# Kernel optimization log

Hardware: AMD Instinct MI355X
Metric: run time of the kernel (lower is better)

## Reference

```python
import jax, jax.numpy as jnp
import numpy as np

HIDDEN = 4096
N_HEADS = 32
N_KV_HEADS = 8
HEAD_DIM = 128
ROPE_BASE = 10000.0


def setup_inputs() -> dict:
    key = jax.random.key(0)
    k1, k2, k3, k4, k5 = jax.random.split(key, 5)
    s = 0.02  # init scale for weights
    return {
        "hidden_states": jax.random.normal(k1, (1, 2048, HIDDEN), dtype=jnp.float32),
        "Wq": jax.random.normal(k2, (N_HEADS * HEAD_DIM, HIDDEN), dtype=jnp.float32) * s,
        "Wk": jax.random.normal(k3, (N_KV_HEADS * HEAD_DIM, HIDDEN), dtype=jnp.float32) * s,
        "Wv": jax.random.normal(k4, (N_KV_HEADS * HEAD_DIM, HIDDEN), dtype=jnp.float32) * s,
        "Wo": jax.random.normal(k5, (HIDDEN, HIDDEN), dtype=jnp.float32) * s,
    }


def _rope(x, cos, sin):
    # x: [B, H, T, D]; cos/sin: [T, D/2] -> rotate split halves (Llama style)
    d2 = x.shape[-1] // 2
    x1, x2 = x[..., :d2], x[..., d2:]
    return jnp.concatenate([x1 * cos - x2 * sin, x1 * sin + x2 * cos], axis=-1)


def reference(hidden_states, Wq, Wk, Wv, Wo):
    B, T, _ = hidden_states.shape
    H, Hkv, D = N_HEADS, N_KV_HEADS, HEAD_DIM
    G = H // Hkv  # kv groups

    q = jnp.einsum("bth,qh->btq", hidden_states, Wq).reshape(B, T, H, D).transpose(0, 2, 1, 3)
    k = jnp.einsum("bth,kh->btk", hidden_states, Wk).reshape(B, T, Hkv, D).transpose(0, 2, 1, 3)
    v = jnp.einsum("bth,vh->btv", hidden_states, Wv).reshape(B, T, Hkv, D).transpose(0, 2, 1, 3)

    # RoPE (position_offset = 0)
    positions = jnp.arange(T, dtype=jnp.float32)
    inv_freq = ROPE_BASE ** (-jnp.arange(0, D, 2, dtype=jnp.float32) / D)  # [D/2]
    angles = positions[:, None] * inv_freq[None, :]                        # [T, D/2]
    cos, sin = jnp.cos(angles), jnp.sin(angles)
    q = _rope(q, cos, sin)
    k = _rope(k, cos, sin)

    # GQA attention without materializing expanded K/V: group query heads
    qg = q.reshape(B, Hkv, G, T, D)
    scale = 1.0 / jnp.sqrt(jnp.asarray(D, dtype=q.dtype))
    scores = jnp.einsum("bkgtd,bksd->bkgts", qg, k) * scale  # [B, Hkv, G, T, T]
    causal = jnp.tril(jnp.ones((T, T), dtype=bool))
    scores = jnp.where(causal, scores, jnp.finfo(scores.dtype).min)
    probs = jax.nn.softmax(scores, axis=-1)
    attn = jnp.einsum("bkgts,bksd->bkgtd", probs, v)          # [B, Hkv, G, T, D]
    attn = attn.reshape(B, H, T, D).transpose(0, 2, 1, 3).reshape(B, T, H * D)

    return jnp.einsum("btq,oq->bto", attn, Wo)
```

## Files before the change

kernel.cpp:

```cpp
#include <hip/hip_runtime.h>
#include <stdint.h>

#define T_SEQ   2048
#define HID     4096
#define NH      32
#define NKV     8
#define HD      128
#define QCOLS   6144
#define QK_SCALE 0.08838834764831845f

typedef _Float16 half_t;
typedef _Float16 half8 __attribute__((ext_vector_type(8)));
typedef _Float16 half4v __attribute__((ext_vector_type(4)));
typedef float    f32x4 __attribute__((ext_vector_type(4)));

typedef __attribute__((address_space(1))) const void cg_void;
typedef __attribute__((address_space(3))) void lds_void;

__global__ __launch_bounds__(256) void cast_f32_f16_k(const float* __restrict__ in,
                                                      half_t* __restrict__ out, int n4) {
  int i = blockIdx.x * 256 + threadIdx.x;
  if (i >= n4) return;
  f32x4 v = *(const f32x4*)(in + (size_t)i * 4);
  half4v o;
  o[0] = (half_t)v[0]; o[1] = (half_t)v[1]; o[2] = (half_t)v[2]; o[3] = (half_t)v[3];
  *(half4v*)(out + (size_t)i * 4) = o;
}

__global__ __launch_bounds__(256) void rope_tables_k(float* __restrict__ cs) {
  int idx = blockIdx.x * 256 + threadIdx.x;
  int t = idx >> 6, i = idx & 63;
  float inv = expf(-(float)i * 0.14391156831212787f);
  float a = (float)t * inv;
  cs[idx] = cosf(a);
  cs[131072 + idx] = sinf(a);
}

__global__ __launch_bounds__(256) void rope_apply_k(half_t* __restrict__ QKV,
                                                    const float* __restrict__ cs) {
  int idx = blockIdx.x * 256 + threadIdx.x;
  int i = idx & 63;
  int rem = idx >> 6;
  int head = rem % 40;
  int t = rem / 40;
  int colbase = (head < 32) ? head * HD : HID + (head - 32) * HD;
  size_t base = (size_t)t * QCOLS + colbase;
  float c = cs[t * 64 + i], s = cs[131072 + t * 64 + i];
  float x1 = (float)QKV[base + i];
  float x2 = (float)QKV[base + 64 + i];
  float o1 = x1 * c - x2 * s;
  float o2 = x1 * s + x2 * c;
  if (head < 32) { o1 *= QK_SCALE; o2 *= QK_SCALE; }
  QKV[base + i]      = (half_t)o1;
  QKV[base + 64 + i] = (half_t)o2;
}

__global__ __launch_bounds__(256) void transpose_v_k(const half_t* __restrict__ QKV,
                                                     half_t* __restrict__ Vt) {
  int idx = blockIdx.x * 256 + threadIdx.x;
  int d  = idx & 127;
  int ts = (idx >> 7) & 255;
  int kh = idx >> 15;
  half8 o;
#pragma unroll
  for (int i = 0; i < 8; ++i)
    o[i] = QKV[(size_t)(ts * 8 + i) * QCOLS + HID + NKV * HD + kh * HD + d];
  *(half8*)&Vt[(size_t)kh * (HD * T_SEQ) + (size_t)d * T_SEQ + ts * 8] = o;
}

template <int OUT_HALF>
__global__ __launch_bounds__(256) void gemm_bt(const half_t* __restrict__ A,
                                               const half_t* __restrict__ B,
                                               void* __restrict__ Cout,
                                               int M, int N, int K) {
  __shared__ half_t Alds[128 * 64];
  __shared__ half_t Blds[128 * 64];
  const int nwg = gridDim.x;
  const int q8 = nwg >> 3;
  const int bid = blockIdx.x;
  const int swz = (bid & 7) * q8 + (bid >> 3);
  const int nbm = M >> 7;
  const int row0 = (swz % nbm) * 128;
  const int col0 = (swz / nbm) * 128;
  const int tid  = threadIdx.x;
  const int lane = tid & 63;
  const int wid  = tid >> 6;
  const int wr = wid >> 1, wc = wid & 1;
  const int lr = lane & 15, hi = lane >> 4;

  f32x4 acc[4][4] = {};

  for (int k0 = 0; k0 < K; k0 += 64) {
#pragma unroll
    for (int c = 0; c < 4; ++c) {
      int idx = c * 256 + tid;
      int r = idx >> 3, s = idx & 7;
      int cc = s ^ (r & 7);
      int base = (c * 256 + wid * 64) * 8;
      __builtin_amdgcn_global_load_lds(
          (cg_void*)(A + (size_t)(row0 + r) * K + k0 + cc * 8),
          (lds_void*)(&Alds[base]), 16, 0, 0);
      __builtin_amdgcn_global_load_lds(
          (cg_void*)(B + (size_t)(col0 + r) * K + k0 + cc * 8),
          (lds_void*)(&Blds[base]), 16, 0, 0);
    }
    __syncthreads();
#pragma unroll
    for (int kk = 0; kk < 2; ++kk) {
      half8 af[4], bf[4];
#pragma unroll
      for (int mi = 0; mi < 4; ++mi) {
        int ra = wr * 64 + mi * 16 + lr;
        int slot = (kk * 4 + hi) ^ (ra & 7);
        af[mi] = *(const half8*)&Alds[ra * 64 + slot * 8];
      }
#pragma unroll
      for (int ni = 0; ni < 4; ++ni) {
        int rb = wc * 64 + ni * 16 + lr;
        int slot = (kk * 4 + hi) ^ (rb & 7);
        bf[ni] = *(const half8*)&Blds[rb * 64 + slot * 8];
      }
#pragma unroll
      for (int mi = 0; mi < 4; ++mi)
#pragma unroll
        for (int ni = 0; ni < 4; ++ni)
          acc[mi][ni] = __builtin_amdgcn_mfma_f32_16x16x32_f16(af[mi], bf[ni], acc[mi][ni], 0, 0, 0);
    }
    __syncthreads();
  }

#pragma unroll
  for (int mi = 0; mi < 4; ++mi)
#pragma unroll
    for (int ni = 0; ni < 4; ++ni)
#pragma unroll
      for (int r = 0; r < 4; ++r) {
        int row = row0 + wr * 64 + mi * 16 + hi * 4 + r;
        int col = col0 + wc * 64 + ni * 16 + lr;
        float v = acc[mi][ni][r];
        if (OUT_HALF) ((half_t*)Cout)[(size_t)row * N + col] = (half_t)v;
        else          ((float*)Cout)[(size_t)row * N + col] = v;
      }
}

__global__ __launch_bounds__(256) void attn_k(const half_t* __restrict__ QKV,
                                              const half_t* __restrict__ Vt,
                                              half_t* __restrict__ Ob) {
  const int bid = blockIdx.x;
  const int qb = 31 - (bid >> 5);
  const int h  = bid & 31;
  const int kh = h >> 2;
  const int tid = threadIdx.x;
  const int lane = tid & 63;
  const int w = tid >> 6;
  const int lr = lane & 15, hi = lane >> 4;
  const int qrow = qb * 64 + w * 16;

  __shared__ half_t Klds[64 * 128];
  __shared__ half_t Vlds[128 * 64];
  __shared__ half_t Plds[4 * 16 * 72];

  const half_t* Qp  = QKV + h * HD;
  const half_t* Kp  = QKV + HID + kh * HD;
  const half_t* Vtp = Vt + (size_t)kh * (HD * T_SEQ);

  half8 qf[4];
#pragma unroll
  for (int kk = 0; kk < 4; ++kk)
    qf[kk] = *(const half8*)&Qp[(size_t)(qrow + lr) * QCOLS + kk * 32 + hi * 8];

  f32x4 acc[8] = {};
  float mrow[4], lrow[4];
#pragma unroll
  for (int r = 0; r < 4; ++r) { mrow[r] = -1e30f; lrow[r] = 0.0f; }

  half_t* Pw = &Plds[w * (16 * 72)];
  const int nt = qb + 1;
  for (int t = 0; t < nt; ++t) {
    const int kv0 = t * 64;
#pragma unroll
    for (int c = 0; c < 4; ++c) {
      int chunk = c * 256 + tid;
      int r = chunk >> 4, s = chunk & 15;
      int cc = (s & 8) | ((s ^ r) & 7);
      __builtin_amdgcn_global_load_lds(
          (cg_void*)(Kp + (size_t)(kv0 + r) * QCOLS + cc * 8),
          (lds_void*)(&Klds[(c * 256 + w * 64) * 8]), 16, 0, 0);
    }
#pragma unroll
    for (int c = 0; c < 4; ++c) {
      int chunk = c * 256 + tid;
      int r = chunk >> 3, s = chunk & 7;
      int cc = (s ^ r) & 7;
      __builtin_amdgcn_global_load_lds(
          (cg_void*)(Vtp + (size_t)r * T_SEQ + kv0 + cc * 8),
          (lds_void*)(&Vlds[(c * 256 + w * 64) * 8]), 16, 0, 0);
    }
    __syncthreads();

    f32x4 s[4] = {};
#pragma unroll
    for (int jt = 0; jt < 4; ++jt)
#pragma unroll
      for (int kk = 0; kk < 4; ++kk) {
        int srow = jt * 16 + lr;
        int sl = kk * 4 + hi;
        int c = (sl & 8) | ((sl ^ srow) & 7);
        half8 kf = *(const half8*)&Klds[srow * 128 + c * 8];
        s[jt] = __builtin_amdgcn_mfma_f32_16x16x32_f16(qf[kk], kf, s[jt], 0, 0, 0);
      }

    if (t == qb) {
#pragma unroll
      for (int jt = 0; jt < 4; ++jt)
#pragma unroll
        for (int r = 0; r < 4; ++r) {
          int ig = qrow + hi * 4 + r;
          int jg = kv0 + jt * 16 + lr;
          if (jg > ig) s[jt][r] = -1e30f;
        }
    }

    float mx[4], scl[4], ls[4];
#pragma unroll
    for (int r = 0; r < 4; ++r)
      mx[r] = fmaxf(fmaxf(s[0][r], s[1][r]), fmaxf(s[2][r], s[3][r]));
#pragma unroll
    for (int off = 1; off < 16; off <<= 1)
#pragma unroll
      for (int r = 0; r < 4; ++r)
        mx[r] = fmaxf(mx[r], __shfl_xor(mx[r], off, 64));
#pragma unroll
    for (int r = 0; r < 4; ++r) {
      float mn = fmaxf(mrow[r], mx[r]);
      scl[r] = __expf(mrow[r] - mn);
      mrow[r] = mn;
      ls[r] = 0.0f;
#pragma unroll
      for (int jt = 0; jt < 4; ++jt) {
        s[jt][r] = __expf(s[jt][r] - mn);
        ls[r] += s[jt][r];
      }
    }
#pragma unroll
    for (int off = 1; off < 16; off <<= 1)
#pragma unroll
      for (int r = 0; r < 4; ++r)
        ls[r] += __shfl_xor(ls[r], off, 64);
#pragma unroll
    for (int r = 0; r < 4; ++r) lrow[r] = lrow[r] * scl[r] + ls[r];
#pragma unroll
    for (int g = 0; g < 8; ++g)
#pragma unroll
      for (int r = 0; r < 4; ++r) acc[g][r] *= scl[r];

#pragma unroll
    for (int jt = 0; jt < 4; ++jt)
#pragma unroll
      for (int r = 0; r < 4; ++r)
        Pw[(hi * 4 + r) * 72 + jt * 16 + lr] = (half_t)s[jt][r];
    half8 pf[2];
#pragma unroll
    for (int jt = 0; jt < 2; ++jt)
      pf[jt] = *(const half8*)&Pw[lr * 72 + jt * 32 + hi * 8];

#pragma unroll
    for (int g = 0; g < 8; ++g)
#pragma unroll
      for (int jt = 0; jt < 2; ++jt) {
        int vrow = g * 16 + lr;
        int sl = jt * 4 + hi;
        int c = (sl ^ vrow) & 7;
        half8 vf = *(const half8*)&Vlds[vrow * 64 + c * 8];
        acc[g] = __builtin_amdgcn_mfma_f32_16x16x32_f16(pf[jt], vf, acc[g], 0, 0, 0);
      }
    __syncthreads();
  }

#pragma unroll
  for (int g = 0; g < 8; ++g)
#pragma unroll
    for (int r = 0; r < 4; ++r) {
      int row = qrow + hi * 4 + r;
      int col = h * HD + g * 16 + lr;
      Ob[(size_t)row * HID + col] = (half_t)(acc[g][r] / lrow[r]);
    }
}

extern "C" void kernel_launch(void* const* d_in, const int* in_sizes, int n_in,
                              void* d_out, int out_size, void* d_ws, size_t ws_size,
                              hipStream_t stream) {
  const float* hs = (const float*)d_in[0];
  const float* Wq = (const float*)d_in[1];
  const float* Wk = (const float*)d_in[2];
  const float* Wv = (const float*)d_in[3];
  const float* Wo = (const float*)d_in[4];
  float* out = (float*)d_out;

  char* ws = (char*)d_ws;
  half_t* Xh    = (half_t*)(ws + 0);
  half_t* Vt    = (half_t*)(ws + 0);
  half_t* Wqkvh = (half_t*)(ws + 16777216);
  half_t* Woh   = (half_t*)(ws + 67108864);
  half_t* QKV   = (half_t*)(ws + 100663296);
  half_t* attnh = (half_t*)(ws + 125829120);
  float*  cs    = (float*)(ws + 142606336);
  if (ws_size < 143654912ull) return;

  cast_f32_f16_k<<<8192, 256, 0, stream>>>(hs, Xh, 2097152);
  cast_f32_f16_k<<<16384, 256, 0, stream>>>(Wq, Wqkvh, 4194304);
  cast_f32_f16_k<<<4096, 256, 0, stream>>>(Wk, Wqkvh + 16777216, 1048576);
  cast_f32_f16_k<<<4096, 256, 0, stream>>>(Wv, Wqkvh + 20971520, 1048576);
  cast_f32_f16_k<<<16384, 256, 0, stream>>>(Wo, Woh, 4194304);
  rope_tables_k<<<512, 256, 0, stream>>>(cs);

  gemm_bt<1><<<768, 256, 0, stream>>>(Xh, Wqkvh, (void*)QKV, 2048, 6144, 4096);
  rope_apply_k<<<20480, 256, 0, stream>>>(QKV, cs);
  transpose_v_k<<<1024, 256, 0, stream>>>(QKV, Vt);
  attn_k<<<1024, 256, 0, stream>>>(QKV, Vt, attnh);
  gemm_bt<0><<<512, 256, 0, stream>>>(attnh, Woh, (void*)out, 2048, 4096, 4096);
}
```

Measured before the change: 365.0 us.

## Replace GEMMs with double-buffered 8-wave ping-pong kernel and fuse cast launches

Replaces the single-buffered 128x128 GEMM with an 8-wave kernel that double-buffers LDS, prefetches the next K tile while computing the current one, and splits MFMA work into barrier-separated phases with raised scheduling priority. Tile sizes become 256x192 for the QKV projection and 128x256 for the output projection, giving 256 workgroups each. The five separate fp32-to-fp16 cast launches are merged into one kernel that picks its source by index range. This aims to hide global load latency and raise MFMA utilisation, at the cost of more LDS and register pressure per workgroup.

```diff
diff --git a/kernel.cpp b/kernel.cpp
--- a/kernel.cpp
+++ b/kernel.cpp
@@ -17,14 +17,25 @@
 typedef __attribute__((address_space(1))) const void cg_void;
 typedef __attribute__((address_space(3))) void lds_void;
 
-__global__ __launch_bounds__(256) void cast_f32_f16_k(const float* __restrict__ in,
-                                                      half_t* __restrict__ out, int n4) {
+__global__ __launch_bounds__(256) void cast_all_k(const float* __restrict__ X,
+                                                  const float* __restrict__ Wq,
+                                                  const float* __restrict__ Wk,
+                                                  const float* __restrict__ Wv,
+                                                  const float* __restrict__ Wo,
+                                                  half_t* __restrict__ Xh,
+                                                  half_t* __restrict__ Wqkvh,
+                                                  half_t* __restrict__ Woh) {
   int i = blockIdx.x * 256 + threadIdx.x;
-  if (i >= n4) return;
-  f32x4 v = *(const f32x4*)(in + (size_t)i * 4);
+  const float* src; half_t* dst; int off;
+  if (i < 2097152)      { src = X;  dst = Xh;               off = i; }
+  else if (i < 6291456) { src = Wq; dst = Wqkvh;            off = i - 2097152; }
+  else if (i < 7340032) { src = Wk; dst = Wqkvh + 16777216; off = i - 6291456; }
+  else if (i < 8388608) { src = Wv; dst = Wqkvh + 20971520; off = i - 7340032; }
+  else                  { src = Wo; dst = Woh;              off = i - 8388608; }
+  f32x4 v = *(const f32x4*)(src + (size_t)off * 4);
   half4v o;
   o[0] = (half_t)v[0]; o[1] = (half_t)v[1]; o[2] = (half_t)v[2]; o[3] = (half_t)v[3];
-  *(half4v*)(out + (size_t)i * 4) = o;
+  *(half4v*)(dst + (size_t)off * 4) = o;
 }
 
 __global__ __launch_bounds__(256) void rope_tables_k(float* __restrict__ cs) {
@@ -68,76 +79,114 @@
   *(half8*)&Vt[(size_t)kh * (HD * T_SEQ) + (size_t)d * T_SEQ + ts * 8] = o;
 }
 
-template <int OUT_HALF>
-__global__ __launch_bounds__(256) void gemm_bt(const half_t* __restrict__ A,
-                                               const half_t* __restrict__ B,
-                                               void* __restrict__ Cout,
-                                               int M, int N, int K) {
-  __shared__ half_t Alds[128 * 64];
-  __shared__ half_t Blds[128 * 64];
-  const int nwg = gridDim.x;
-  const int q8 = nwg >> 3;
+template <int BM, int BN, int OUT_HALF>
+__global__ __launch_bounds__(512, 2) void gemm8p_k(const half_t* __restrict__ A,
+                                                   const half_t* __restrict__ Bm,
+                                                   void* __restrict__ Cout,
+                                                   int M, int N, int K) {
+  constexpr int MF = BM / 32;
+  constexpr int NF = BN / 64;
+  constexpr int MH = MF / 2;
+  constexpr int LA = BM / 64;
+  constexpr int LB = BN / 64;
+  __shared__ half_t Al[2][BM * 64];
+  __shared__ half_t Bl[2][BN * 64];
+
+  const int nbm = M / BM;
+  const int nwg = nbm * (N / BN);
   const int bid = blockIdx.x;
-  const int swz = (bid & 7) * q8 + (bid >> 3);
-  const int nbm = M >> 7;
-  const int row0 = (swz % nbm) * 128;
-  const int col0 = (swz / nbm) * 128;
-  const int tid  = threadIdx.x;
-  const int lane = tid & 63;
-  const int wid  = tid >> 6;
-  const int wr = wid >> 1, wc = wid & 1;
+  const int swz = (bid & 7) * (nwg >> 3) + (bid >> 3);
+  const int brow = (swz % nbm) * BM;
+  const int bcol = (swz / nbm) * BN;
+  const int tid = threadIdx.x;
+  const int lane = tid & 63, wid = tid >> 6;
+  const int wr = wid >> 2, wc = wid & 3;
   const int lr = lane & 15, hi = lane >> 4;
-
-  f32x4 acc[4][4] = {};
-
-  for (int k0 = 0; k0 < K; k0 += 64) {
-#pragma unroll
-    for (int c = 0; c < 4; ++c) {
-      int idx = c * 256 + tid;
-      int r = idx >> 3, s = idx & 7;
-      int cc = s ^ (r & 7);
-      int base = (c * 256 + wid * 64) * 8;
-      __builtin_amdgcn_global_load_lds(
-          (cg_void*)(A + (size_t)(row0 + r) * K + k0 + cc * 8),
-          (lds_void*)(&Alds[base]), 16, 0, 0);
-      __builtin_amdgcn_global_load_lds(
-          (cg_void*)(B + (size_t)(col0 + r) * K + k0 + cc * 8),
-          (lds_void*)(&Blds[base]), 16, 0, 0);
-    }
-    __syncthreads();
-#pragma unroll
-    for (int kk = 0; kk < 2; ++kk) {
-      half8 af[4], bf[4];
-#pragma unroll
-      for (int mi = 0; mi < 4; ++mi) {
-        int ra = wr * 64 + mi * 16 + lr;
-        int slot = (kk * 4 + hi) ^ (ra & 7);
-        af[mi] = *(const half8*)&Alds[ra * 64 + slot * 8];
-      }
-#pragma unroll
-      for (int ni = 0; ni < 4; ++ni) {
-        int rb = wc * 64 + ni * 16 + lr;
-        int slot = (kk * 4 + hi) ^ (rb & 7);
-        bf[ni] = *(const half8*)&Blds[rb * 64 + slot * 8];
-      }
-#pragma unroll
-      for (int mi = 0; mi < 4; ++mi)
-#pragma unroll
-        for (int ni = 0; ni < 4; ++ni)
-          acc[mi][ni] = __builtin_amdgcn_mfma_f32_16x16x32_f16(af[mi], bf[ni], acc[mi][ni], 0, 0, 0);
-    }
-    __syncthreads();
+  const int wrow = wr * (MF * 16), wcol = wc * (NF * 16);
+
+  const half_t* Ab = A + (size_t)brow * K;
+  const half_t* Bb = Bm + (size_t)bcol * K;
+
+  f32x4 acc[MF][NF] = {};
+  half8 afr[MH], bfr[NF];
+
+#define STAGE_A(l, k0, buf) { \
+    int c_ = (l) * 512 + tid; int r_ = c_ >> 3, s_ = c_ & 7; \
+    __builtin_amdgcn_global_load_lds( \
+      (cg_void*)(Ab + (size_t)r_ * K + (k0) + ((s_ ^ (r_ & 7)) * 8)), \
+      (lds_void*)(&Al[buf][((l) * 512 + wid * 64) * 8]), 16, 0, 0); }
+#define STAGE_B(l, k0, buf) { \
+    int c_ = (l) * 512 + tid; int r_ = c_ >> 3, s_ = c_ & 7; \
+    __builtin_amdgcn_global_load_lds( \
+      (cg_void*)(Bb + (size_t)r_ * K + (k0) + ((s_ ^ (r_ & 7)) * 8)), \
+      (lds_void*)(&Bl[buf][((l) * 512 + wid * 64) * 8]), 16, 0, 0); }
+#define RD_A(i, mh, kk, buf) { \
+    int row_ = wrow + ((mh) * MH + (i)) * 16 + lr; int ks_ = (kk) * 4 + hi; \
+    afr[i] = *(const half8*)&Al[buf][row_ * 64 + ((ks_ ^ (row_ & 7)) * 8)]; }
+#define RD_B(n, kk, buf) { \
+    int row_ = wcol + (n) * 16 + lr; int ks_ = (kk) * 4 + hi; \
+    bfr[n] = *(const half8*)&Bl[buf][row_ * 64 + ((ks_ ^ (row_ & 7)) * 8)]; }
+#define MFMA_PH(mh) { \
+    __builtin_amdgcn_s_setprio(1); \
+    _Pragma("unroll") for (int i_ = 0; i_ < MH; ++i_) \
+      _Pragma("unroll") for (int n_ = 0; n_ < NF; ++n_) \
+        acc[(mh) * MH + i_][n_] = __builtin_amdgcn_mfma_f32_16x16x32_f16( \
+            afr[i_], bfr[n_], acc[(mh) * MH + i_][n_], 0, 0, 0); \
+    __builtin_amdgcn_s_setprio(0); }
+
+#define DO_TILE(T, BUF) { \
+    const int kn_ = ((T) + 1) * 64; const bool pf_ = ((T) + 1) < NT; \
+     \
+    if (pf_) { _Pragma("unroll") for (int l_ = 0; l_ < LA; ++l_) STAGE_A(l_, kn_, (BUF) ^ 1); } \
+    _Pragma("unroll") for (int n_ = 0; n_ < NF; ++n_) RD_B(n_, 0, BUF); \
+    _Pragma("unroll") for (int i_ = 0; i_ < MH; ++i_) RD_A(i_, 0, 0, BUF); \
+    MFMA_PH(0); \
+    __builtin_amdgcn_s_barrier(); __builtin_amdgcn_sched_barrier(0); \
+     \
+    if (pf_) { _Pragma("unroll") for (int l_ = 0; l_ < LB; ++l_) STAGE_B(l_, kn_, (BUF) ^ 1); } \
+    _Pragma("unroll") for (int i_ = 0; i_ < MH; ++i_) RD_A(i_, 1, 0, BUF); \
+    MFMA_PH(1); \
+    __builtin_amdgcn_s_barrier(); __builtin_amdgcn_sched_barrier(0); \
+     \
+    _Pragma("unroll") for (int n_ = 0; n_ < NF; ++n_) RD_B(n_, 1, BUF); \
+    _Pragma("unroll") for (int i_ = 0; i_ < MH; ++i_) RD_A(i_, 1, 1, BUF); \
+    MFMA_PH(1); \
+    __builtin_amdgcn_s_barrier(); __builtin_amdgcn_sched_barrier(0); \
+     \
+    _Pragma("unroll") for (int i_ = 0; i_ < MH; ++i_) RD_A(i_, 0, 1, BUF); \
+    MFMA_PH(0); \
+    asm volatile("s_waitcnt vmcnt(0)" ::: "memory"); \
+    __syncthreads(); }
+
+  const int NT = K / 64;
+#pragma unroll
+  for (int l_ = 0; l_ < LA; ++l_) STAGE_A(l_, 0, 0);
+#pragma unroll
+  for (int l_ = 0; l_ < LB; ++l_) STAGE_B(l_, 0, 0);
+  asm volatile("s_waitcnt vmcnt(0)" ::: "memory");
+  __syncthreads();
+
+  for (int t = 0; t < NT; t += 2) {
+    DO_TILE(t, 0);
+    DO_TILE(t + 1, 1);
   }
 
-#pragma unroll
-  for (int mi = 0; mi < 4; ++mi)
-#pragma unroll
-    for (int ni = 0; ni < 4; ++ni)
+#undef STAGE_A
+#undef STAGE_B
+#undef RD_A
+#undef RD_B
+#undef MFMA_PH
+#undef DO_TILE
+
+#pragma unroll
+  for (int m = 0; m < MF; ++m)
+#pragma unroll
+    for (int n = 0; n < NF; ++n)
 #pragma unroll
       for (int r = 0; r < 4; ++r) {
-        int row = row0 + wr * 64 + mi * 16 + hi * 4 + r;
-        int col = col0 + wc * 64 + ni * 16 + lr;
-        float v = acc[mi][ni][r];
+        int row = brow + wrow + m * 16 + hi * 4 + r;
+        int col = bcol + wcol + n * 16 + lr;
+        float v = acc[m][n][r];
         if (OUT_HALF) ((half_t*)Cout)[(size_t)row * N + col] = (half_t)v;
         else          ((float*)Cout)[(size_t)row * N + col] = v;
       }
@@ -307,16 +356,12 @@
   float*  cs    = (float*)(ws + 142606336);
   if (ws_size < 143654912ull) return;
 
-  cast_f32_f16_k<<<8192, 256, 0, stream>>>(hs, Xh, 2097152);
-  cast_f32_f16_k<<<16384, 256, 0, stream>>>(Wq, Wqkvh, 4194304);
-  cast_f32_f16_k<<<4096, 256, 0, stream>>>(Wk, Wqkvh + 16777216, 1048576);
-  cast_f32_f16_k<<<4096, 256, 0, stream>>>(Wv, Wqkvh + 20971520, 1048576);
-  cast_f32_f16_k<<<16384, 256, 0, stream>>>(Wo, Woh, 4194304);
+  cast_all_k<<<49152, 256, 0, stream>>>(hs, Wq, Wk, Wv, Wo, Xh, Wqkvh, Woh);
   rope_tables_k<<<512, 256, 0, stream>>>(cs);
 
-  gemm_bt<1><<<768, 256, 0, stream>>>(Xh, Wqkvh, (void*)QKV, 2048, 6144, 4096);
+  gemm8p_k<256, 192, 1><<<256, 512, 0, stream>>>(Xh, Wqkvh, (void*)QKV, 2048, 6144, 4096);
   rope_apply_k<<<20480, 256, 0, stream>>>(QKV, cs);
   transpose_v_k<<<1024, 256, 0, stream>>>(QKV, Vt);
   attn_k<<<1024, 256, 0, stream>>>(QKV, Vt, attnh);
-  gemm_bt<0><<<512, 256, 0, stream>>>(attnh, Woh, (void*)out, 2048, 4096, 4096);
-}
+  gemm8p_k<128, 256, 0><<<256, 512, 0, stream>>>(attnh, Woh, (void*)out, 2048, 4096, 4096);
+}
```

New measurement: 336.0 us. -7.9%, faster.
